# Kernel tuning notes

Hardware: AMD Instinct MI355X
Metric: run time of the kernel (lower is better)

## Reference

```python
import jax, jax.numpy as jnp
import numpy as np

B, D = 8192, 1024

def setup_inputs() -> dict:
    key = jax.random.key(0)
    ks = jax.random.split(key, 5)
    scale = 1.0 / np.sqrt(D)
    return {
        "x": jax.random.normal(ks[0], (B, D), dtype=jnp.float32),
        "h": jax.random.normal(ks[1], (B, D), dtype=jnp.float32),
        "c": jax.random.normal(ks[2], (B, D), dtype=jnp.float32),
        # gate order: [input, forget, output, candidate]
        "Wx": jax.random.normal(ks[3], (4, D, D), dtype=jnp.float32) * scale,
        "Wh": jax.random.normal(ks[4], (4, D, D), dtype=jnp.float32) * scale,
    }

def reference(x, h, c, Wx, Wh):
    # two batched GEMMs covering all 8 projections: [B,D] x [4,D,D] -> [4,B,D]
    gx = jnp.einsum('bd,gdk->gbk', x, Wx)
    gh = jnp.einsum('bd,gdk->gbk', h, Wh)
    g = gx + gh
    i = jax.nn.sigmoid(g[0])
    f = jax.nn.sigmoid(g[1])
    o = jax.nn.sigmoid(g[2])
    u = jnp.tanh(g[3])
    c_t = i * u + f * c
    h_t = o * jnp.tanh(c_t)
    return (h_t, c_t)
```

## Files before the change

kernel.cpp:

```cpp
#include <hip/hip_runtime.h>
#include <hip/hip_bf16.h>
#include <cstdint>


#define LDS_SLOT  49152
#define LDS_TOTAL 147456

typedef __attribute__((ext_vector_type(8))) short bf16x8;
typedef __attribute__((ext_vector_type(4))) float f32x4;
typedef __attribute__((ext_vector_type(4))) unsigned int u32x4;

static __device__ __forceinline__ unsigned short f2bf(float f) {
  union { float f; unsigned int u; } v; v.f = f;
  unsigned int u = v.u;
  unsigned int r = (u + 0x7FFFu + ((u >> 16) & 1u)) >> 16;
  return (unsigned short)r;
}

static __device__ __forceinline__ void load16(const void* gp, void* lp) {
  __builtin_amdgcn_global_load_lds(
      (const __attribute__((address_space(1))) void*)gp,
      (__attribute__((address_space(3))) void*)lp, 16, 0, 0);
}

static __device__ __forceinline__ float sigmoid_f(float x) {
  return 1.0f / (1.0f + __expf(-x));
}
static __device__ __forceinline__ float tanh_f(float x) {
  float e = __expf(-2.0f * fabsf(x));
  float r = (1.0f - e) / (1.0f + e);
  return copysignf(r, x);
}

__global__ __launch_bounds__(256) void pack_a_kernel(
    const float* __restrict__ x, const float* __restrict__ h,
    unsigned short* __restrict__ Apack) {
  int t = blockIdx.x * 256 + threadIdx.x;
  size_t base = (size_t)t * 8;
  int b = (int)(base >> 11);
  int k = (int)(base & 2047);
  const float* src = (k < 1024) ? (x + (size_t)b * 1024 + k)
                                : (h + (size_t)b * 1024 + (k - 1024));
  float4 v0 = ((const float4*)src)[0];
  float4 v1 = ((const float4*)src)[1];
  union { unsigned short s[8]; u32x4 v; } o;
  o.s[0] = f2bf(v0.x); o.s[1] = f2bf(v0.y); o.s[2] = f2bf(v0.z); o.s[3] = f2bf(v0.w);
  o.s[4] = f2bf(v1.x); o.s[5] = f2bf(v1.y); o.s[6] = f2bf(v1.z); o.s[7] = f2bf(v1.w);
  *(u32x4*)(Apack + base) = o.v;
}

__global__ __launch_bounds__(256) void prep_w_kernel(
    const float* __restrict__ Wx, const float* __restrict__ Wh,
    unsigned short* __restrict__ Wt) {
  __shared__ float tile[32][33];
  int bid = blockIdx.x;
  int g = bid >> 11;
  int rem = bid & 2047;
  int kt = rem >> 5;
  int nt = rem & 31;
  int k0 = kt * 32, n0 = nt * 32;
  int tx = threadIdx.x & 31, ty = threadIdx.x >> 5;
  const float* Wsrc;
  int ks;
  if (k0 < 1024) { Wsrc = Wx + (size_t)g * 1048576; ks = k0; }
  else           { Wsrc = Wh + (size_t)g * 1048576; ks = k0 - 1024; }
  #pragma unroll
  for (int s = 0; s < 4; ++s) {
    int r = ty + s * 8;
    tile[r][tx] = Wsrc[(size_t)(ks + r) * 1024 + n0 + tx];
  }
  __syncthreads();
  #pragma unroll
  for (int s = 0; s < 4; ++s) {
    int r = ty + s * 8;
    Wt[(size_t)((g << 10) + n0 + r) * 2048 + k0 + tx] = f2bf(tile[tx][r]);
  }
}

__global__ __launch_bounds__(512, 2) void lstm_gemm_kernel(
    const unsigned short* __restrict__ Apack,
    const unsigned short* __restrict__ Wt,
    const float* __restrict__ cprev,
    float* __restrict__ out) {
  extern __shared__ char lds[];
  const int tid = threadIdx.x;
  const int l = tid & 63;
  const int w = tid >> 6;
  const int wr = w >> 2;
  const int wc = w & 3;
  const int bid = blockIdx.x;
  const int mt = bid >> 4;
  const int nt = bid & 15;
  const int m0 = mt << 7;
  const int n0 = nt << 6;

  f32x4 acc[4][4];
  #pragma unroll
  for (int mf = 0; mf < 4; ++mf)
    #pragma unroll
    for (int g = 0; g < 4; ++g) acc[mf][g] = (f32x4)0.0f;

  auto stage = [&](int slot, int t) {
    const int k0 = t << 6;
    char* base = lds + slot * LDS_SLOT;
    #pragma unroll
    for (int j = 0; j < 2; ++j) {
      int c = j * 512 + tid;
      int Dd = c << 4;
      int row = Dd >> 7;
      int kbs = (Dd & 127) ^ ((row & 7) << 4);
      const unsigned short* gp = Apack + (size_t)(m0 + row) * 2048 + k0 + (kbs >> 1);
      load16(gp, base + ((c & ~63) << 4));
    }
    #pragma unroll
    for (int g = 0; g < 4; ++g) {
      int Dd = tid << 4;
      int row = Dd >> 7;
      int kbs = (Dd & 127) ^ ((row & 7) << 4);
      const unsigned short* gp =
          Wt + (size_t)((g << 10) + n0 + row) * 2048 + k0 + (kbs >> 1);
      load16(gp, base + 16384 + (g << 13) + ((tid & ~63) << 4));
    }
  };

  const int lr = l & 15;
  const int kgrp = (l >> 4) << 4;
  const int arow = wr * 64 + lr;
  const int brow = wc * 16 + lr;
  const int sxr = (lr & 7) << 4;

  stage(0, 0);
  stage(1, 1);

  int sc = 0;
  #pragma unroll 1
  for (int t = 0; t < 32; ++t) {
    if (t < 31) asm volatile("s_waitcnt vmcnt(6)" ::: "memory");
    else        asm volatile("s_waitcnt vmcnt(0)" ::: "memory");
    __builtin_amdgcn_sched_barrier(0);
    __builtin_amdgcn_s_barrier();
    __builtin_amdgcn_sched_barrier(0);
    if (t + 2 < 32) {
      int sn = sc + 2; if (sn >= 3) sn -= 3;
      stage(sn, t + 2);
    }
    __builtin_amdgcn_sched_barrier(0);
    const char* Ab = lds + sc * LDS_SLOT;
    const char* Bb = Ab + 16384;
    #pragma unroll
    for (int kk = 0; kk < 2; ++kk) {
      const int kbs = (kk * 64 + kgrp) ^ sxr;
      bf16x8 a0 = *(const bf16x8*)(Ab + (arow     ) * 128 + kbs);
      bf16x8 a1 = *(const bf16x8*)(Ab + (arow + 16) * 128 + kbs);
      bf16x8 a2 = *(const bf16x8*)(Ab + (arow + 32) * 128 + kbs);
      bf16x8 a3 = *(const bf16x8*)(Ab + (arow + 48) * 128 + kbs);
      bf16x8 b0 = *(const bf16x8*)(Bb +         brow * 128 + kbs);
      bf16x8 b1 = *(const bf16x8*)(Bb +  8192 + brow * 128 + kbs);
      bf16x8 b2 = *(const bf16x8*)(Bb + 16384 + brow * 128 + kbs);
      bf16x8 b3 = *(const bf16x8*)(Bb + 24576 + brow * 128 + kbs);
      __builtin_amdgcn_s_setprio(1);
      acc[0][0] = __builtin_amdgcn_mfma_f32_16x16x32_bf16(a0, b0, acc[0][0], 0, 0, 0);
      acc[0][1] = __builtin_amdgcn_mfma_f32_16x16x32_bf16(a0, b1, acc[0][1], 0, 0, 0);
      acc[0][2] = __builtin_amdgcn_mfma_f32_16x16x32_bf16(a0, b2, acc[0][2], 0, 0, 0);
      acc[0][3] = __builtin_amdgcn_mfma_f32_16x16x32_bf16(a0, b3, acc[0][3], 0, 0, 0);
      acc[1][0] = __builtin_amdgcn_mfma_f32_16x16x32_bf16(a1, b0, acc[1][0], 0, 0, 0);
      acc[1][1] = __builtin_amdgcn_mfma_f32_16x16x32_bf16(a1, b1, acc[1][1], 0, 0, 0);
      acc[1][2] = __builtin_amdgcn_mfma_f32_16x16x32_bf16(a1, b2, acc[1][2], 0, 0, 0);
      acc[1][3] = __builtin_amdgcn_mfma_f32_16x16x32_bf16(a1, b3, acc[1][3], 0, 0, 0);
      acc[2][0] = __builtin_amdgcn_mfma_f32_16x16x32_bf16(a2, b0, acc[2][0], 0, 0, 0);
      acc[2][1] = __builtin_amdgcn_mfma_f32_16x16x32_bf16(a2, b1, acc[2][1], 0, 0, 0);
      acc[2][2] = __builtin_amdgcn_mfma_f32_16x16x32_bf16(a2, b2, acc[2][2], 0, 0, 0);
      acc[2][3] = __builtin_amdgcn_mfma_f32_16x16x32_bf16(a2, b3, acc[2][3], 0, 0, 0);
      acc[3][0] = __builtin_amdgcn_mfma_f32_16x16x32_bf16(a3, b0, acc[3][0], 0, 0, 0);
      acc[3][1] = __builtin_amdgcn_mfma_f32_16x16x32_bf16(a3, b1, acc[3][1], 0, 0, 0);
      acc[3][2] = __builtin_amdgcn_mfma_f32_16x16x32_bf16(a3, b2, acc[3][2], 0, 0, 0);
      acc[3][3] = __builtin_amdgcn_mfma_f32_16x16x32_bf16(a3, b3, acc[3][3], 0, 0, 0);
      __builtin_amdgcn_s_setprio(0);
      __builtin_amdgcn_sched_barrier(0);
    }
    sc += 1; if (sc >= 3) sc -= 3;
  }

  const int q = (l >> 4) << 2;
  const int col = n0 + wc * 16 + lr;
  #pragma unroll
  for (int mf = 0; mf < 4; ++mf) {
    #pragma unroll
    for (int j = 0; j < 4; ++j) {
      int row = m0 + wr * 64 + mf * 16 + q + j;
      float gi = acc[mf][0][j];
      float gf = acc[mf][1][j];
      float go = acc[mf][2][j];
      float gu = acc[mf][3][j];
      float i_ = sigmoid_f(gi);
      float f_ = sigmoid_f(gf);
      float o_ = sigmoid_f(go);
      float u_ = tanh_f(gu);
      size_t idx = (size_t)row * 1024 + col;
      float ct = i_ * u_ + f_ * cprev[idx];
      float ht = o_ * tanh_f(ct);
      out[idx] = ht;
      out[8388608 + idx] = ct;
    }
  }
}

extern "C" void kernel_launch(void* const* d_in, const int* in_sizes, int n_in,
                              void* d_out, int out_size, void* d_ws, size_t ws_size,
                              hipStream_t stream) {
  const float* x  = (const float*)d_in[0];
  const float* h  = (const float*)d_in[1];
  const float* c  = (const float*)d_in[2];
  const float* Wx = (const float*)d_in[3];
  const float* Wh = (const float*)d_in[4];
  float* out = (float*)d_out;

  unsigned short* Apack = (unsigned short*)d_ws;
  unsigned short* Wt = (unsigned short*)((char*)d_ws + 33554432);

  hipFuncSetAttribute((const void*)lstm_gemm_kernel,
                      hipFuncAttributeMaxDynamicSharedMemorySize, LDS_TOTAL);

  pack_a_kernel<<<8192, 256, 0, stream>>>(x, h, Apack);
  prep_w_kernel<<<8192, 256, 0, stream>>>(Wx, Wh, Wt);
  lstm_gemm_kernel<<<dim3(1024), dim3(512), LDS_TOTAL, stream>>>(Apack, Wt, c, out);
}
```

Baseline: 175.9 us.

## Double M tile to 256 rows with 8-phase ping-pong LDS pipeline

Each workgroup now covers 256 rows instead of 128, with 4x4 gate columns per wave, so each B tile is reused across twice as many rows. The old triple-buffered stage is replaced by two 64KB buffers. Each k-step is split into four quarter MFMA phases, and the next A/B loads are interleaved between barriers. Block IDs are remapped so neighbouring blocks share A/B panels in cache. This raises accumulator register pressure (128 acc floats per lane), halves the grid to 512 blocks, and adds many more barriers per k-step.

Result: slower. 180.5 us (+2.6%).

```diff
diff --git a/kernel.cpp b/kernel.cpp
--- a/kernel.cpp
+++ b/kernel.cpp
@@ -3,8 +3,7 @@
 #include <cstdint>
 
 
-#define LDS_SLOT  49152
-#define LDS_TOTAL 147456
+#define LDS_TOTAL 131072
 
 typedef __attribute__((ext_vector_type(8))) short bf16x8;
 typedef __attribute__((ext_vector_type(4))) float f32x4;
@@ -88,106 +87,143 @@
   const int w = tid >> 6;
   const int wr = w >> 2;
   const int wc = w & 3;
-  const int bid = blockIdx.x;
+  const int bid0 = blockIdx.x;
+  const int bid = (bid0 & 7) * 64 + (bid0 >> 3);
   const int mt = bid >> 4;
   const int nt = bid & 15;
-  const int m0 = mt << 7;
+  const int m0 = mt << 8;
   const int n0 = nt << 6;
 
-  f32x4 acc[4][4];
-  #pragma unroll
-  for (int mf = 0; mf < 4; ++mf)
+  char* const buf0 = lds;
+  char* const buf1 = lds + 65536;
+
+  f32x4 acc[8][4];
+  #pragma unroll
+  for (int mf = 0; mf < 8; ++mf)
     #pragma unroll
     for (int g = 0; g < 4; ++g) acc[mf][g] = (f32x4)0.0f;
 
-  auto stage = [&](int slot, int t) {
-    const int k0 = t << 6;
-    char* base = lds + slot * LDS_SLOT;
+  bf16x8 aR[4][2];
+  bf16x8 bR[4][2];
+
+  const int lr = l & 15;
+  const int kgrp = (l >> 4) << 4;
+  const int sx = (lr & 7) << 4;
+  const int aoff = (wr * 128 + lr) * 128;
+  const int boff = 32768 + (wc * 16 + lr) * 128;
+
+  auto stageA = [&](char* bufb, int h, int kstep) {
+    const int k0 = kstep << 6;
     #pragma unroll
     for (int j = 0; j < 2; ++j) {
       int c = j * 512 + tid;
-      int Dd = c << 4;
-      int row = Dd >> 7;
-      int kbs = (Dd & 127) ^ ((row & 7) << 4);
-      const unsigned short* gp = Apack + (size_t)(m0 + row) * 2048 + k0 + (kbs >> 1);
-      load16(gp, base + ((c & ~63) << 4));
+      int byt = c << 4;
+      int rl = byt >> 7;
+      int kb = (byt & 127) ^ ((rl & 7) << 4);
+      const unsigned short* gp =
+          Apack + (size_t)(m0 + h * 128 + rl) * 2048 + k0 + (kb >> 1);
+      load16(gp, bufb + h * 16384 + ((c & ~63) << 4));
     }
-    #pragma unroll
-    for (int g = 0; g < 4; ++g) {
-      int Dd = tid << 4;
-      int row = Dd >> 7;
-      int kbs = (Dd & 127) ^ ((row & 7) << 4);
+  };
+  auto stageB = [&](char* bufb, int h, int kstep) {
+    const int k0 = kstep << 6;
+    #pragma unroll
+    for (int j = 0; j < 2; ++j) {
+      int c = j * 512 + tid;
+      int byt = c << 4;
+      int g = 2 * h + (byt >> 13);
+      int loc = byt & 8191;
+      int rl = loc >> 7;
+      int kb = (loc & 127) ^ ((rl & 7) << 4);
       const unsigned short* gp =
-          Wt + (size_t)((g << 10) + n0 + row) * 2048 + k0 + (kbs >> 1);
-      load16(gp, base + 16384 + (g << 13) + ((tid & ~63) << 4));
+          Wt + (size_t)((g << 10) + n0 + rl) * 2048 + k0 + (kb >> 1);
+      load16(gp, bufb + 32768 + h * 16384 + ((c & ~63) << 4));
     }
   };
 
-  const int lr = l & 15;
-  const int kgrp = (l >> 4) << 4;
-  const int arow = wr * 64 + lr;
-  const int brow = wc * 16 + lr;
-  const int sxr = (lr & 7) << 4;
-
-  stage(0, 0);
-  stage(1, 1);
-
-  int sc = 0;
+  auto readA = [&](const char* bufc, int mh) {
+    #pragma unroll
+    for (int i = 0; i < 4; ++i)
+      #pragma unroll
+      for (int kk = 0; kk < 2; ++kk)
+        aR[i][kk] = *(const bf16x8*)(bufc + aoff + (mh * 64 + i * 16) * 128 +
+                                     ((kk * 64 + kgrp) ^ sx));
+  };
+  auto readB = [&](const char* bufc, int gh) {
+    #pragma unroll
+    for (int i = 0; i < 2; ++i)
+      #pragma unroll
+      for (int kk = 0; kk < 2; ++kk)
+        bR[gh * 2 + i][kk] = *(const bf16x8*)(bufc + boff + (gh * 2 + i) * 8192 +
+                                              ((kk * 64 + kgrp) ^ sx));
+  };
+  auto mfma16 = [&](int mh, int gh) {
+    __builtin_amdgcn_s_setprio(1);
+    #pragma unroll
+    for (int kk = 0; kk < 2; ++kk)
+      #pragma unroll
+      for (int i = 0; i < 4; ++i)
+        #pragma unroll
+        for (int gg = 0; gg < 2; ++gg)
+          acc[mh * 4 + i][gh * 2 + gg] = __builtin_amdgcn_mfma_f32_16x16x32_bf16(
+              aR[i][kk], bR[gh * 2 + gg][kk], acc[mh * 4 + i][gh * 2 + gg], 0, 0, 0);
+    __builtin_amdgcn_s_setprio(0);
+  };
+
+  stageA(buf0, 0, 0); stageA(buf0, 1, 0);
+  stageB(buf0, 0, 0); stageB(buf0, 1, 0);
+  stageB(buf1, 0, 1); stageB(buf1, 1, 1);
+  stageA(buf1, 0, 1);
+  asm volatile("s_waitcnt vmcnt(6)" ::: "memory");
+  __builtin_amdgcn_sched_barrier(0);
+  __builtin_amdgcn_s_barrier();
+
+  auto kstep = [&](int t, char* bufc, char* bufn) {
+    readA(bufc, 0);
+    readB(bufc, 0);
+    if (t + 1 < 32) stageA(bufn, 1, t + 1);
+    asm volatile("s_waitcnt lgkmcnt(8)" ::: "memory");
+    __builtin_amdgcn_s_barrier();
+    asm volatile("s_waitcnt lgkmcnt(0)" ::: "memory");
+    __builtin_amdgcn_sched_barrier(0);
+    mfma16(0, 0);
+    __builtin_amdgcn_s_barrier();
+    readB(bufc, 1);
+    if (t + 2 < 32) stageB(bufc, 0, t + 2);
+    __builtin_amdgcn_s_barrier();
+    asm volatile("s_waitcnt lgkmcnt(0)" ::: "memory");
+    __builtin_amdgcn_sched_barrier(0);
+    mfma16(0, 1);
+    __builtin_amdgcn_s_barrier();
+    readA(bufc, 1);
+    if (t + 2 < 32) stageB(bufc, 1, t + 2);
+    __builtin_amdgcn_s_barrier();
+    asm volatile("s_waitcnt lgkmcnt(0)" ::: "memory");
+    __builtin_amdgcn_sched_barrier(0);
+    mfma16(1, 1);
+    __builtin_amdgcn_s_barrier();
+    if (t + 2 < 32) stageA(bufc, 0, t + 2);
+    if (t < 30) asm volatile("s_waitcnt vmcnt(6)" ::: "memory");
+    else        asm volatile("s_waitcnt vmcnt(0)" ::: "memory");
+    __builtin_amdgcn_sched_barrier(0);
+    __builtin_amdgcn_s_barrier();
+    mfma16(1, 0);
+    __builtin_amdgcn_s_barrier();
+  };
+
   #pragma unroll 1
-  for (int t = 0; t < 32; ++t) {
-    if (t < 31) asm volatile("s_waitcnt vmcnt(6)" ::: "memory");
-    else        asm volatile("s_waitcnt vmcnt(0)" ::: "memory");
-    __builtin_amdgcn_sched_barrier(0);
-    __builtin_amdgcn_s_barrier();
-    __builtin_amdgcn_sched_barrier(0);
-    if (t + 2 < 32) {
-      int sn = sc + 2; if (sn >= 3) sn -= 3;
-      stage(sn, t + 2);
-    }
-    __builtin_amdgcn_sched_barrier(0);
-    const char* Ab = lds + sc * LDS_SLOT;
-    const char* Bb = Ab + 16384;
-    #pragma unroll
-    for (int kk = 0; kk < 2; ++kk) {
-      const int kbs = (kk * 64 + kgrp) ^ sxr;
-      bf16x8 a0 = *(const bf16x8*)(Ab + (arow     ) * 128 + kbs);
-      bf16x8 a1 = *(const bf16x8*)(Ab + (arow + 16) * 128 + kbs);
-      bf16x8 a2 = *(const bf16x8*)(Ab + (arow + 32) * 128 + kbs);
-      bf16x8 a3 = *(const bf16x8*)(Ab + (arow + 48) * 128 + kbs);
-      bf16x8 b0 = *(const bf16x8*)(Bb +         brow * 128 + kbs);
-      bf16x8 b1 = *(const bf16x8*)(Bb +  8192 + brow * 128 + kbs);
-      bf16x8 b2 = *(const bf16x8*)(Bb + 16384 + brow * 128 + kbs);
-      bf16x8 b3 = *(const bf16x8*)(Bb + 24576 + brow * 128 + kbs);
-      __builtin_amdgcn_s_setprio(1);
-      acc[0][0] = __builtin_amdgcn_mfma_f32_16x16x32_bf16(a0, b0, acc[0][0], 0, 0, 0);
-      acc[0][1] = __builtin_amdgcn_mfma_f32_16x16x32_bf16(a0, b1, acc[0][1], 0, 0, 0);
-      acc[0][2] = __builtin_amdgcn_mfma_f32_16x16x32_bf16(a0, b2, acc[0][2], 0, 0, 0);
-      acc[0][3] = __builtin_amdgcn_mfma_f32_16x16x32_bf16(a0, b3, acc[0][3], 0, 0, 0);
-      acc[1][0] = __builtin_amdgcn_mfma_f32_16x16x32_bf16(a1, b0, acc[1][0], 0, 0, 0);
-      acc[1][1] = __builtin_amdgcn_mfma_f32_16x16x32_bf16(a1, b1, acc[1][1], 0, 0, 0);
-      acc[1][2] = __builtin_amdgcn_mfma_f32_16x16x32_bf16(a1, b2, acc[1][2], 0, 0, 0);
-      acc[1][3] = __builtin_amdgcn_mfma_f32_16x16x32_bf16(a1, b3, acc[1][3], 0, 0, 0);
-      acc[2][0] = __builtin_amdgcn_mfma_f32_16x16x32_bf16(a2, b0, acc[2][0], 0, 0, 0);
-      acc[2][1] = __builtin_amdgcn_mfma_f32_16x16x32_bf16(a2, b1, acc[2][1], 0, 0, 0);
-      acc[2][2] = __builtin_amdgcn_mfma_f32_16x16x32_bf16(a2, b2, acc[2][2], 0, 0, 0);
-      acc[2][3] = __builtin_amdgcn_mfma_f32_16x16x32_bf16(a2, b3, acc[2][3], 0, 0, 0);
-      acc[3][0] = __builtin_amdgcn_mfma_f32_16x16x32_bf16(a3, b0, acc[3][0], 0, 0, 0);
-      acc[3][1] = __builtin_amdgcn_mfma_f32_16x16x32_bf16(a3, b1, acc[3][1], 0, 0, 0);
-      acc[3][2] = __builtin_amdgcn_mfma_f32_16x16x32_bf16(a3, b2, acc[3][2], 0, 0, 0);
-      acc[3][3] = __builtin_amdgcn_mfma_f32_16x16x32_bf16(a3, b3, acc[3][3], 0, 0, 0);
-      __builtin_amdgcn_s_setprio(0);
-      __builtin_amdgcn_sched_barrier(0);
-    }
-    sc += 1; if (sc >= 3) sc -= 3;
+  for (int tt = 0; tt < 16; ++tt) {
+    kstep(2 * tt,     buf0, buf1);
+    kstep(2 * tt + 1, buf1, buf0);
   }
 
   const int q = (l >> 4) << 2;
   const int col = n0 + wc * 16 + lr;
   #pragma unroll
-  for (int mf = 0; mf < 4; ++mf) {
+  for (int mf = 0; mf < 8; ++mf) {
     #pragma unroll
     for (int j = 0; j < 4; ++j) {
-      int row = m0 + wr * 64 + mf * 16 + q + j;
+      int row = m0 + wr * 128 + mf * 16 + q + j;
       float gi = acc[mf][0][j];
       float gf = acc[mf][1][j];
       float go = acc[mf][2][j];
@@ -223,5 +259,5 @@
 
   pack_a_kernel<<<8192, 256, 0, stream>>>(x, h, Apack);
   prep_w_kernel<<<8192, 256, 0, stream>>>(Wx, Wh, Wt);
-  lstm_gemm_kernel<<<dim3(1024), dim3(512), LDS_TOTAL, stream>>>(Apack, Wt, c, out);
-}
+  lstm_gemm_kernel<<<dim3(512), dim3(512), LDS_TOTAL, stream>>>(Apack, Wt, c, out);
+}
```
